# Kernel optimization log

Measured on AMD Instinct MI355X. Metric: run time of the kernel, lower is better.

The kernel has to match this reference:

```python
import jax, jax.numpy as jnp
import numpy as np

N, E, F_IN, D, H = 20000, 640000, 128, 16, 8  # nodes, edges, in_features, out_features, n_heads


def _linear_params(k, fan_in, fan_out):
    W = jax.random.normal(k, (fan_in, fan_out), jnp.float32) / np.sqrt(fan_in)
    b = jnp.zeros((fan_out,), jnp.float32)
    return W, b


def setup_inputs() -> dict:
    key = jax.random.key(0)
    ks = jax.random.split(key, 8)
    x = jax.random.normal(ks[0], (N, F_IN), jnp.float32)
    edge_index = jax.random.randint(ks[1], (2, E), 0, N, dtype=jnp.int64)
    Wq, bq = _linear_params(ks[2], F_IN, D * H)
    Wk, bk = _linear_params(ks[3], F_IN, D * H)
    Wv, bv = _linear_params(ks[4], F_IN, D * H)
    Wpsi, bpsi = _linear_params(ks[5], D, D)
    Wo, bo = _linear_params(ks[6], D * H * 2, F_IN)
    gamma = jnp.ones((F_IN,), jnp.float32)
    beta = jnp.zeros((F_IN,), jnp.float32)
    return {"x": x, "edge_index": edge_index, "Wq": Wq, "bq": bq, "Wk": Wk, "bk": bk,
            "Wv": Wv, "bv": bv, "Wpsi": Wpsi, "bpsi": bpsi, "Wo": Wo, "bo": bo,
            "gamma": gamma, "beta": beta}


def _segment_softmax(logits, seg, num_segments):
    # numerically-stable softmax of edge logits grouped by destination node (row)
    m = jax.ops.segment_max(logits, seg, num_segments=num_segments)  # [N,H]
    m = jnp.where(jnp.isfinite(m), m, 0.0)
    e = jnp.exp(logits - m[seg])  # [E,H]
    s = jax.ops.segment_sum(e, seg, num_segments=num_segments)  # [N,H]
    return e / (s[seg] + 1e-16)


def reference(x, edge_index, Wq, bq, Wk, bk, Wv, bv, Wpsi, bpsi, Wo, bo, gamma, beta):
    q = (x @ Wq + bq).reshape(N, H, D)
    k = (x @ Wk + bk).reshape(N, H, D)
    v = (x @ Wv + bv).reshape(N, H, D)
    row, col = edge_index[0], edge_index[1]

    logits = jnp.einsum('ehd,ehd->eh', q[row], k[col]) / np.sqrt(D)  # [E,H]
    alpha = _segment_softmax(logits, row, N)  # [E,H]

    v_j = v[col]  # [E,H,D]
    h_lp = jax.ops.segment_sum((alpha[..., None] * v_j).reshape(E, H * D), row, num_segments=N)
    v_bp = jnp.tanh(v_j @ Wpsi + bpsi)  # per-head linear on last dim, [E,H,D]
    h_bp = jax.ops.segment_sum((alpha[..., None] * v_bp).reshape(E, H * D), row, num_segments=N)

    h_out = jnp.concatenate([h_lp, h_bp], axis=1) @ Wo + bo  # [N,F_IN]
    y = x + jax.nn.relu(h_out)
    mu = jnp.mean(y, axis=-1, keepdims=True)
    var = jnp.mean(jnp.square(y - mu), axis=-1, keepdims=True)
    return (y - mu) * jax.lax.rsqrt(var + 1e-5) * gamma + beta
```

## Files before the change

### kernel.cpp

```cpp
#include <hip/hip_runtime.h>
#include <hip/hip_bf16.h>
#include <math.h>

#define NN 20000
#define EE 640000
#define NCH 8
#define CHN 2500
#define SLOT 24

typedef __attribute__((ext_vector_type(8))) short short8;
typedef __attribute__((ext_vector_type(4))) float f32x4;
typedef __hip_bfloat16 bf16;
typedef __hip_bfloat162 bf162;

__device__ inline ushort f2bf(float f) {
  bf16 h = __float2bfloat16(f);
  return *(ushort*)&h;
}
__device__ inline float2 ldbf2(const ushort* p) {
  return __bfloat1622float2(*(const bf162*)p);
}
__device__ inline float2 bf2u(uint u) {
  return __bfloat1622float2(*(const bf162*)&u);
}
__device__ inline float fast_tanh(float x) {
  float xx = fminf(fmaxf(x, -9.0f), 9.0f);
  float e = exp2f(xx * 2.885390082f);
  return (e - 1.0f) * __builtin_amdgcn_rcpf(e + 1.0f);
}


__global__ __launch_bounds__(256) void qkv_mfma(
    const float* __restrict__ x,
    const float* __restrict__ Wq, const float* __restrict__ bq,
    const float* __restrict__ Wk, const float* __restrict__ bk,
    const float* __restrict__ Wv, const float* __restrict__ bv,
    const float* __restrict__ Wpsi, const float* __restrict__ bpsi,
    float* __restrict__ qbuf, ushort* __restrict__ kvb,
    int* __restrict__ cursor2) {
  __shared__ ushort As[128 * 136];
  __shared__ ushort Bts[128 * 136];
  __shared__ float Wps[256];
  __shared__ float bps[16];
  int t = threadIdx.x;
  {
    int flat = (blockIdx.y * 157 + blockIdx.x) * 256 + t;
    for (int j = flat; j < NN * NCH; j += 157 * 3 * 256) cursor2[j] = 0;
  }
  int n0 = blockIdx.x * 128;
  int mat = blockIdx.y;
  const float* W    = mat == 0 ? Wq : (mat == 1 ? Wk : Wv);
  const float* bias = mat == 0 ? bq : (mat == 1 ? bk : bv);
  if (mat == 2) {
    Wps[t] = Wpsi[t];
    if (t < 16) bps[t] = bpsi[t];
  }

  {
    int r = t >> 1, half = (t & 1) * 64;
    int n = n0 + r;
    ushort* dst = &As[r * 136 + half];
    if (n < NN) {
      const float* src = x + (size_t)n * 128 + half;
#pragma unroll
      for (int j = 0; j < 8; ++j) {
        float4 f0 = *(const float4*)(src + 8 * j);
        float4 f1 = *(const float4*)(src + 8 * j + 4);
        ushort tmp[8] = {f2bf(f0.x), f2bf(f0.y), f2bf(f0.z), f2bf(f0.w),
                         f2bf(f1.x), f2bf(f1.y), f2bf(f1.z), f2bf(f1.w)};
        *(uint4*)(dst + 8 * j) = *(uint4*)tmp;
      }
    } else {
#pragma unroll
      for (int j = 0; j < 8; ++j) *(uint4*)(dst + 8 * j) = make_uint4(0, 0, 0, 0);
    }
  }
  {
    int k = t >> 1, nh = (t & 1) * 64;
    const float* src = W + (size_t)k * 128 + nh;
#pragma unroll
    for (int i = 0; i < 16; ++i) {
      float4 f = *(const float4*)(src + 4 * i);
      Bts[(nh + 4 * i + 0) * 136 + k] = f2bf(f.x);
      Bts[(nh + 4 * i + 1) * 136 + k] = f2bf(f.y);
      Bts[(nh + 4 * i + 2) * 136 + k] = f2bf(f.z);
      Bts[(nh + 4 * i + 3) * 136 + k] = f2bf(f.w);
    }
  }
  __syncthreads();

  int w = t >> 6, lane = t & 63;
  int m = lane & 15, q = lane >> 4;
  int r0 = w * 32;
  f32x4 acc0[8], acc1[8];
#pragma unroll
  for (int c = 0; c < 8; ++c) {
    acc0[c] = (f32x4){0.f, 0.f, 0.f, 0.f};
    acc1[c] = (f32x4){0.f, 0.f, 0.f, 0.f};
  }
#pragma unroll
  for (int kb = 0; kb < 4; ++kb) {
    int kof = kb * 32 + 8 * q;
    short8 a0 = *(const short8*)&As[(r0 + m) * 136 + kof];
    short8 a1 = *(const short8*)&As[(r0 + 16 + m) * 136 + kof];
#pragma unroll
    for (int c = 0; c < 8; ++c) {
      short8 b = *(const short8*)&Bts[(c * 16 + m) * 136 + kof];
      acc0[c] = __builtin_amdgcn_mfma_f32_16x16x32_bf16(a0, b, acc0[c], 0, 0, 0);
      acc1[c] = __builtin_amdgcn_mfma_f32_16x16x32_bf16(a1, b, acc1[c], 0, 0, 0);
    }
  }
  if (mat == 2) __syncthreads();

  int koff2 = (mat == 2) ? 4 : 0;
#pragma unroll
  for (int c = 0; c < 8; ++c) {
    int col = c * 16 + m;
    float bb = bias[col];
    size_t pos = (size_t)(c * 4 + (m >> 2)) * 12 + (m & 3) + koff2;
#pragma unroll
    for (int reg = 0; reg < 4; ++reg) {
      int rl0 = r0 + 4 * q + reg;
      int rl1 = rl0 + 16;
      int row0 = n0 + rl0;
      int row1 = n0 + rl1;
      float v0 = acc0[c][reg] + bb;
      float v1 = acc1[c][reg] + bb;
      if (mat == 0) {
        if (row0 < NN) qbuf[(size_t)row0 * 128 + col] = v0;
        if (row1 < NN) qbuf[(size_t)row1 * 128 + col] = v1;
      } else {
        if (row0 < NN) kvb[(size_t)row0 * 384 + pos] = f2bf(v0);
        if (row1 < NN) kvb[(size_t)row1 * 384 + pos] = f2bf(v1);
        if (mat == 2) {
          Bts[rl0 * 136 + col] = f2bf(v0);
          Bts[rl1 * 136 + col] = f2bf(v1);
        }
      }
    }
  }

  if (mat == 2) {
    __syncthreads();
#pragma unroll
    for (int ii = 0; ii < 4; ++ii) {
      int idx = ii * 256 + t;
      int rloc = idx >> 3, h = idx & 7;
      int n = n0 + rloc;
      const ushort* vp = &Bts[rloc * 136 + h * 16];
      uint4 a = *(const uint4*)vp;
      uint4 b = *(const uint4*)(vp + 8);
      float v[16];
      {
        float2 f;
        f = bf2u(a.x); v[0] = f.x;  v[1] = f.y;
        f = bf2u(a.y); v[2] = f.x;  v[3] = f.y;
        f = bf2u(a.z); v[4] = f.x;  v[5] = f.y;
        f = bf2u(a.w); v[6] = f.x;  v[7] = f.y;
        f = bf2u(b.x); v[8] = f.x;  v[9] = f.y;
        f = bf2u(b.y); v[10] = f.x; v[11] = f.y;
        f = bf2u(b.z); v[12] = f.x; v[13] = f.y;
        f = bf2u(b.w); v[14] = f.x; v[15] = f.y;
      }
      float o[16];
#pragma unroll
      for (int d = 0; d < 16; ++d) o[d] = bps[d];
#pragma unroll
      for (int dp = 0; dp < 16; ++dp) {
        float vv = v[dp];
#pragma unroll
        for (int d = 0; d < 16; ++d) o[d] = fmaf(vv, Wps[dp * 16 + d], o[d]);
      }
      if (n < NN) {
        ushort* dst = kvb + (size_t)n * 384;
#pragma unroll
        for (int j = 0; j < 8; ++j) {
          uint u = (uint)f2bf(fast_tanh(o[2 * j])) |
                   ((uint)f2bf(fast_tanh(o[2 * j + 1])) << 16);
          int grp = h * 4 + (j >> 1);
          int within = (2 * j) & 3;
          *(uint*)(dst + grp * 12 + 8 + within) = u;
        }
      }
    }
  }
}

__global__ __launch_bounds__(256) void scatter_kernel(
    const int* __restrict__ ei,
    int* __restrict__ cursor2, ushort* __restrict__ scol2) {
  int e = blockIdx.x * 256 + threadIdx.x;
  if (e < EE) {
    int r = ei[e];
    int c = ei[EE + e];
    int ch = c / CHN;
    int pos = atomicAdd(&cursor2[r * NCH + ch], 1);
    if (pos < SLOT) scol2[(r * NCH + ch) * SLOT + pos] = (ushort)c;
  }
}

__global__ __launch_bounds__(256) void aggregate_kernel(
    const float* __restrict__ qbuf, const ushort* __restrict__ kvb,
    const int* __restrict__ cursor2, const ushort* __restrict__ scol2,
    ushort* __restrict__ hbufb) {
  int t = threadIdx.x;
  int lane = t & 63;
  int wid = __builtin_amdgcn_readfirstlane(t >> 6);
  int wg = blockIdx.x * 4 + wid;
  int n0 = wg * 2;
  int l31 = lane & 31;
  int half = lane >> 5;
  const float SC = 0.25f * 1.44269504f;

  float4 q0 = *(const float4*)(qbuf + (size_t)n0 * 128 + l31 * 4);
  float4 q1 = *(const float4*)(qbuf + (size_t)(n0 + 1) * 128 + l31 * 4);
  q0.x *= SC; q0.y *= SC; q0.z *= SC; q0.w *= SC;
  q1.x *= SC; q1.y *= SC; q1.z *= SC; q1.w *= SC;

  int mycnt = cursor2[n0 * NCH + (lane & 15)];

  float s0 = 0.f, s1 = 0.f;
  float4 aV0 = make_float4(0.f, 0.f, 0.f, 0.f), aV1 = aV0;
  float4 aB0 = aV0, aB1 = aV0;

  const char* kvc = (const char*)kvb;
  uint lo24 = (uint)l31 * 24u;

  for (int ch = 0; ch < NCH; ++ch) {
#pragma unroll
    for (int ni = 0; ni < 2; ++ni) {
      int cnt = __builtin_amdgcn_readfirstlane(__shfl(mycnt, ni * NCH + ch));
      cnt = cnt > SLOT ? SLOT : cnt;
      if (cnt == 0) continue;
      const uint* slu = (const uint*)(scol2 + ((n0 + ni) * NCH + ch) * SLOT);
      float4 q = ni ? q1 : q0;
      float ls = 0.f;
      float4 lV = make_float4(0.f, 0.f, 0.f, 0.f);
      float4 lB = make_float4(0.f, 0.f, 0.f, 0.f);
      int npair = (cnt + 1) >> 1;
      for (int p = 0; p < npair; ++p) {
        uint wv = slu[p];
        uint e0 = wv & 0xffffu;
        uint e1 = wv >> 16;
        bool pv = (2 * p + 1) < cnt;
        uint e1c = pv ? e1 : e0;
        uint e = half ? e1c : e0;
        const char* pb = kvc + (size_t)e * 768u + lo24;
        uint4 L0 = *(const uint4*)pb;
        uint2 L1 = *(const uint2*)(pb + 16);
        float2 k0 = bf2u(L0.x), k1 = bf2u(L0.y);
        float d = fmaf(q.x, k0.x, fmaf(q.y, k0.y, fmaf(q.z, k1.x, q.w * k1.y)));
        d += __shfl_xor(d, 1);
        d += __shfl_xor(d, 2);
        float wgt = exp2f(d);
        wgt = (half && !pv) ? 0.f : wgt;
        ls += wgt;
        float2 v0 = bf2u(L0.z), v1 = bf2u(L0.w);
        lV.x = fmaf(wgt, v0.x, lV.x); lV.y = fmaf(wgt, v0.y, lV.y);
        lV.z = fmaf(wgt, v1.x, lV.z); lV.w = fmaf(wgt, v1.y, lV.w);
        float2 b0 = bf2u(L1.x), b1 = bf2u(L1.y);
        lB.x = fmaf(wgt, b0.x, lB.x); lB.y = fmaf(wgt, b0.y, lB.y);
        lB.z = fmaf(wgt, b1.x, lB.z); lB.w = fmaf(wgt, b1.y, lB.w);
      }
      if (ni == 0) {
        s0 += ls;
        aV0.x += lV.x; aV0.y += lV.y; aV0.z += lV.z; aV0.w += lV.w;
        aB0.x += lB.x; aB0.y += lB.y; aB0.z += lB.z; aB0.w += lB.w;
      } else {
        s1 += ls;
        aV1.x += lV.x; aV1.y += lV.y; aV1.z += lV.z; aV1.w += lV.w;
        aB1.x += lB.x; aB1.y += lB.y; aB1.z += lB.z; aB1.w += lB.w;
      }
    }
    __syncthreads();
  }

#pragma unroll
  for (int ni = 0; ni < 2; ++ni) {
    float s = ni ? s1 : s0;
    float4 V = ni ? aV1 : aV0;
    float4 B = ni ? aB1 : aB0;
    s += __shfl_xor(s, 32);
    V.x += __shfl_xor(V.x, 32); V.y += __shfl_xor(V.y, 32);
    V.z += __shfl_xor(V.z, 32); V.w += __shfl_xor(V.w, 32);
    B.x += __shfl_xor(B.x, 32); B.y += __shfl_xor(B.y, 32);
    B.z += __shfl_xor(B.z, 32); B.w += __shfl_xor(B.w, 32);
    float inv = s > 0.f ? 1.f / s : 0.f;
    if (half == 0) {
      ushort* hp = hbufb + (size_t)(n0 + ni) * 256 + l31 * 4;
      uint2 uv, ub;
      uv.x = (uint)f2bf(V.x * inv) | ((uint)f2bf(V.y * inv) << 16);
      uv.y = (uint)f2bf(V.z * inv) | ((uint)f2bf(V.w * inv) << 16);
      ub.x = (uint)f2bf(B.x * inv) | ((uint)f2bf(B.y * inv) << 16);
      ub.y = (uint)f2bf(B.z * inv) | ((uint)f2bf(B.w * inv) << 16);
      *(uint2*)(hp)       = uv;
      *(uint2*)(hp + 128) = ub;
    }
  }
}

__global__ __launch_bounds__(256) void output_mfma(
    const ushort* __restrict__ hbufb, const float* __restrict__ x,
    const float* __restrict__ Wo, const float* __restrict__ bo,
    const float* __restrict__ gamma, const float* __restrict__ beta,
    float* __restrict__ out) {
  __shared__ ushort As[128 * 136];
  __shared__ ushort Bts[128 * 136];
  __shared__ float bos[128], gs[128], bts[128];
  int t = threadIdx.x;
  int n0 = blockIdx.x * 128;
  if (t < 128) { bos[t] = bo[t]; gs[t] = gamma[t]; bts[t] = beta[t]; }
  int w = t >> 6, lane = t & 63;
  int m = lane & 15, q = lane >> 4;
  int r0 = w * 32;
  f32x4 acc0[8], acc1[8];
#pragma unroll
  for (int c = 0; c < 8; ++c) {
    acc0[c] = (f32x4){0.f, 0.f, 0.f, 0.f};
    acc1[c] = (f32x4){0.f, 0.f, 0.f, 0.f};
  }
  for (int kc = 0; kc < 2; ++kc) {
    if (kc) __syncthreads();
    {
      int r = t >> 1, half = (t & 1) * 64;
      int n = n0 + r;
      ushort* dst = &As[r * 136 + half];
      if (n < NN) {
        const ushort* src = hbufb + (size_t)n * 256 + kc * 128 + half;
#pragma unroll
        for (int j = 0; j < 8; ++j)
          *(uint4*)(dst + 8 * j) = *(const uint4*)(src + 8 * j);
      } else {
#pragma unroll
        for (int j = 0; j < 8; ++j) *(uint4*)(dst + 8 * j) = make_uint4(0, 0, 0, 0);
      }
    }
    {
      int k = t >> 1, nh = (t & 1) * 64;
      const float* src = Wo + (size_t)(kc * 128 + k) * 128 + nh;
#pragma unroll
      for (int i = 0; i < 16; ++i) {
        float4 f = *(const float4*)(src + 4 * i);
        Bts[(nh + 4 * i + 0) * 136 + k] = f2bf(f.x);
        Bts[(nh + 4 * i + 1) * 136 + k] = f2bf(f.y);
        Bts[(nh + 4 * i + 2) * 136 + k] = f2bf(f.z);
        Bts[(nh + 4 * i + 3) * 136 + k] = f2bf(f.w);
      }
    }
    __syncthreads();
#pragma unroll
    for (int kb = 0; kb < 4; ++kb) {
      int kof = kb * 32 + 8 * q;
      short8 a0 = *(const short8*)&As[(r0 + m) * 136 + kof];
      short8 a1 = *(const short8*)&As[(r0 + 16 + m) * 136 + kof];
#pragma unroll
      for (int c = 0; c < 8; ++c) {
        short8 b = *(const short8*)&Bts[(c * 16 + m) * 136 + kof];
        acc0[c] = __builtin_amdgcn_mfma_f32_16x16x32_bf16(a0, b, acc0[c], 0, 0, 0);
        acc1[c] = __builtin_amdgcn_mfma_f32_16x16x32_bf16(a1, b, acc1[c], 0, 0, 0);
      }
    }
  }
#pragma unroll
  for (int half = 0; half < 2; ++half) {
#pragma unroll
    for (int reg = 0; reg < 4; ++reg) {
      int row = n0 + r0 + half * 16 + 4 * q + reg;
      bool valid = row < NN;
      float vals[8];
      float sum = 0.f;
#pragma unroll
      for (int c = 0; c < 8; ++c) {
        int col = c * 16 + m;
        float a = (half ? acc1[c][reg] : acc0[c][reg]) + bos[col];
        a = fmaxf(a, 0.f);
        float xv = valid ? x[(size_t)row * 128 + col] : 0.f;
        float v = a + xv;
        vals[c] = v;
        sum += v;
      }
      sum += __shfl_xor(sum, 1); sum += __shfl_xor(sum, 2);
      sum += __shfl_xor(sum, 4); sum += __shfl_xor(sum, 8);
      float mean = sum * (1.f / 128.f);
      float ssq = 0.f;
#pragma unroll
      for (int c = 0; c < 8; ++c) {
        float d = vals[c] - mean;
        ssq = fmaf(d, d, ssq);
      }
      ssq += __shfl_xor(ssq, 1); ssq += __shfl_xor(ssq, 2);
      ssq += __shfl_xor(ssq, 4); ssq += __shfl_xor(ssq, 8);
      float rstd = rsqrtf(ssq * (1.f / 128.f) + 1e-5f);
      if (valid) {
#pragma unroll
        for (int c = 0; c < 8; ++c) {
          int col = c * 16 + m;
          out[(size_t)row * 128 + col] = (vals[c] - mean) * rstd * gs[col] + bts[col];
        }
      }
    }
  }
}

extern "C" void kernel_launch(void* const* d_in, const int* in_sizes, int n_in,
                              void* d_out, int out_size, void* d_ws, size_t ws_size,
                              hipStream_t stream) {
  const float* x     = (const float*)d_in[0];
  const int*   ei    = (const int*)d_in[1];
  const float* Wq    = (const float*)d_in[2];
  const float* bq    = (const float*)d_in[3];
  const float* Wk    = (const float*)d_in[4];
  const float* bk    = (const float*)d_in[5];
  const float* Wv    = (const float*)d_in[6];
  const float* bv    = (const float*)d_in[7];
  const float* Wpsi  = (const float*)d_in[8];
  const float* bpsi  = (const float*)d_in[9];
  const float* Wo    = (const float*)d_in[10];
  const float* bo    = (const float*)d_in[11];
  const float* gamma = (const float*)d_in[12];
  const float* beta  = (const float*)d_in[13];
  float* out = (float*)d_out;

  char* ws = (char*)d_ws;
  float*  qbuf    = (float*) (ws);
  ushort* kvb     = (ushort*)(ws + 10240000);
  ushort* hbufb   = (ushort*)(ws + 25600000);
  int*    cursor2 = (int*)   (ws + 35840000);
  ushort* scol2   = (ushort*)(ws + 36480000);

  qkv_mfma<<<dim3(157, 3), 256, 0, stream>>>(x, Wq, bq, Wk, bk, Wv, bv,
                                             Wpsi, bpsi, qbuf, kvb, cursor2);
  scatter_kernel<<<2500, 256, 0, stream>>>(ei, cursor2, scol2);
  aggregate_kernel<<<2500, 256, 0, stream>>>(qbuf, kvb, cursor2, scol2, hbufb);
  output_mfma<<<157, 256, 0, stream>>>(hbufb, x, Wo, bo, gamma, beta, out);
}
```

Baseline: 233.8 us.

## Fuse K and V projections per block, stage kvb rows in LDS, interleave aggregation nodes

Measured after the change: 275.6 us. 1.18x slower.

```diff
diff --git a/kernel.cpp b/kernel.cpp
--- a/kernel.cpp
+++ b/kernel.cpp
@@ -38,20 +38,20 @@
     const float* __restrict__ Wpsi, const float* __restrict__ bpsi,
     float* __restrict__ qbuf, ushort* __restrict__ kvb,
     int* __restrict__ cursor2) {
-  __shared__ ushort As[128 * 136];
-  __shared__ ushort Bts[128 * 136];
+  __shared__ ushort SM[34816];
   __shared__ float Wps[256];
   __shared__ float bps[16];
+  ushort* As = SM;
+  ushort* WB = SM + 17408;
+  ushort* Rs = SM;
   int t = threadIdx.x;
   {
     int flat = (blockIdx.y * 157 + blockIdx.x) * 256 + t;
-    for (int j = flat; j < NN * NCH; j += 157 * 3 * 256) cursor2[j] = 0;
+    for (int j = flat; j < NN * NCH; j += 157 * 2 * 256) cursor2[j] = 0;
   }
   int n0 = blockIdx.x * 128;
   int mat = blockIdx.y;
-  const float* W    = mat == 0 ? Wq : (mat == 1 ? Wk : Wv);
-  const float* bias = mat == 0 ? bq : (mat == 1 ? bk : bv);
-  if (mat == 2) {
+  if (mat == 1) {
     Wps[t] = Wpsi[t];
     if (t < 16) bps[t] = bpsi[t];
   }
@@ -75,92 +75,117 @@
       for (int j = 0; j < 8; ++j) *(uint4*)(dst + 8 * j) = make_uint4(0, 0, 0, 0);
     }
   }
-  {
+  auto stageW = [&](const float* W) {
     int k = t >> 1, nh = (t & 1) * 64;
     const float* src = W + (size_t)k * 128 + nh;
 #pragma unroll
     for (int i = 0; i < 16; ++i) {
       float4 f = *(const float4*)(src + 4 * i);
-      Bts[(nh + 4 * i + 0) * 136 + k] = f2bf(f.x);
-      Bts[(nh + 4 * i + 1) * 136 + k] = f2bf(f.y);
-      Bts[(nh + 4 * i + 2) * 136 + k] = f2bf(f.z);
-      Bts[(nh + 4 * i + 3) * 136 + k] = f2bf(f.w);
-    }
-  }
-  __syncthreads();
+      WB[(nh + 4 * i + 0) * 136 + k] = f2bf(f.x);
+      WB[(nh + 4 * i + 1) * 136 + k] = f2bf(f.y);
+      WB[(nh + 4 * i + 2) * 136 + k] = f2bf(f.z);
+      WB[(nh + 4 * i + 3) * 136 + k] = f2bf(f.w);
+    }
+  };
 
   int w = t >> 6, lane = t & 63;
   int m = lane & 15, q = lane >> 4;
   int r0 = w * 32;
-  f32x4 acc0[8], acc1[8];
+
+  auto runMFMA = [&](f32x4 (&a0)[8], f32x4 (&a1)[8]) {
+#pragma unroll
+    for (int kb = 0; kb < 4; ++kb) {
+      int kof = kb * 32 + 8 * q;
+      short8 x0 = *(const short8*)&As[(r0 + m) * 136 + kof];
+      short8 x1 = *(const short8*)&As[(r0 + 16 + m) * 136 + kof];
+#pragma unroll
+      for (int c = 0; c < 8; ++c) {
+        short8 b = *(const short8*)&WB[(c * 16 + m) * 136 + kof];
+        a0[c] = __builtin_amdgcn_mfma_f32_16x16x32_bf16(x0, b, a0[c], 0, 0, 0);
+        a1[c] = __builtin_amdgcn_mfma_f32_16x16x32_bf16(x1, b, a1[c], 0, 0, 0);
+      }
+    }
+  };
+
+  if (mat == 0) {
+    stageW(Wq);
+    __syncthreads();
+    f32x4 acc0[8], acc1[8];
+#pragma unroll
+    for (int c = 0; c < 8; ++c) {
+      acc0[c] = (f32x4){0.f, 0.f, 0.f, 0.f};
+      acc1[c] = (f32x4){0.f, 0.f, 0.f, 0.f};
+    }
+    runMFMA(acc0, acc1);
+#pragma unroll
+    for (int c = 0; c < 8; ++c) {
+      int col = c * 16 + m;
+      float bb = bq[col];
+#pragma unroll
+      for (int reg = 0; reg < 4; ++reg) {
+        int row0 = n0 + r0 + 4 * q + reg;
+        int row1 = row0 + 16;
+        if (row0 < NN) qbuf[(size_t)row0 * 128 + col] = acc0[c][reg] + bb;
+        if (row1 < NN) qbuf[(size_t)row1 * 128 + col] = acc1[c][reg] + bb;
+      }
+    }
+    return;
+  }
+
+  stageW(Wk);
+  __syncthreads();
+  f32x4 ak0[8], ak1[8], av0[8], av1[8];
 #pragma unroll
   for (int c = 0; c < 8; ++c) {
-    acc0[c] = (f32x4){0.f, 0.f, 0.f, 0.f};
-    acc1[c] = (f32x4){0.f, 0.f, 0.f, 0.f};
-  }
-#pragma unroll
-  for (int kb = 0; kb < 4; ++kb) {
-    int kof = kb * 32 + 8 * q;
-    short8 a0 = *(const short8*)&As[(r0 + m) * 136 + kof];
-    short8 a1 = *(const short8*)&As[(r0 + 16 + m) * 136 + kof];
-#pragma unroll
-    for (int c = 0; c < 8; ++c) {
-      short8 b = *(const short8*)&Bts[(c * 16 + m) * 136 + kof];
-      acc0[c] = __builtin_amdgcn_mfma_f32_16x16x32_bf16(a0, b, acc0[c], 0, 0, 0);
-      acc1[c] = __builtin_amdgcn_mfma_f32_16x16x32_bf16(a1, b, acc1[c], 0, 0, 0);
-    }
-  }
-  if (mat == 2) __syncthreads();
-
-  int koff2 = (mat == 2) ? 4 : 0;
+    ak0[c] = (f32x4){0.f, 0.f, 0.f, 0.f};
+    ak1[c] = (f32x4){0.f, 0.f, 0.f, 0.f};
+    av0[c] = (f32x4){0.f, 0.f, 0.f, 0.f};
+    av1[c] = (f32x4){0.f, 0.f, 0.f, 0.f};
+  }
+  runMFMA(ak0, ak1);
+  __syncthreads();
+  stageW(Wv);
+  __syncthreads();
+  runMFMA(av0, av1);
+  __syncthreads();
+
+  float bbk[8], bbv[8];
 #pragma unroll
   for (int c = 0; c < 8; ++c) {
-    int col = c * 16 + m;
-    float bb = bias[col];
-    size_t pos = (size_t)(c * 4 + (m >> 2)) * 12 + (m & 3) + koff2;
-#pragma unroll
-    for (int reg = 0; reg < 4; ++reg) {
-      int rl0 = r0 + 4 * q + reg;
-      int rl1 = rl0 + 16;
-      int row0 = n0 + rl0;
-      int row1 = n0 + rl1;
-      float v0 = acc0[c][reg] + bb;
-      float v1 = acc1[c][reg] + bb;
-      if (mat == 0) {
-        if (row0 < NN) qbuf[(size_t)row0 * 128 + col] = v0;
-        if (row1 < NN) qbuf[(size_t)row1 * 128 + col] = v1;
-      } else {
-        if (row0 < NN) kvb[(size_t)row0 * 384 + pos] = f2bf(v0);
-        if (row1 < NN) kvb[(size_t)row1 * 384 + pos] = f2bf(v1);
-        if (mat == 2) {
-          Bts[rl0 * 136 + col] = f2bf(v0);
-          Bts[rl1 * 136 + col] = f2bf(v1);
+    bbk[c] = bk[c * 16 + m];
+    bbv[c] = bv[c * 16 + m];
+  }
+
+#pragma unroll
+  for (int hf = 0; hf < 2; ++hf) {
+    if (hf) __syncthreads();
+    if ((w >> 1) == hf) {
+      int rbase = (w & 1) * 32;
+#pragma unroll
+      for (int c = 0; c < 8; ++c) {
+        int gof = (c * 4 + (m >> 2)) * 12 + (m & 3);
+#pragma unroll
+        for (int reg = 0; reg < 4; ++reg) {
+          int rl = rbase + 4 * q + reg;
+          Rs[rl * 392 + gof]            = f2bf(ak0[c][reg] + bbk[c]);
+          Rs[rl * 392 + gof + 4]        = f2bf(av0[c][reg] + bbv[c]);
+          Rs[(rl + 16) * 392 + gof]     = f2bf(ak1[c][reg] + bbk[c]);
+          Rs[(rl + 16) * 392 + gof + 4] = f2bf(av1[c][reg] + bbv[c]);
         }
       }
     }
-  }
-
-  if (mat == 2) {
     __syncthreads();
 #pragma unroll
-    for (int ii = 0; ii < 4; ++ii) {
-      int idx = ii * 256 + t;
-      int rloc = idx >> 3, h = idx & 7;
-      int n = n0 + rloc;
-      const ushort* vp = &Bts[rloc * 136 + h * 16];
-      uint4 a = *(const uint4*)vp;
-      uint4 b = *(const uint4*)(vp + 8);
+    for (int ii = 0; ii < 2; ++ii) {
+      int cell = ii * 256 + t;
+      int rl = cell >> 3, h = cell & 7;
       float v[16];
-      {
-        float2 f;
-        f = bf2u(a.x); v[0] = f.x;  v[1] = f.y;
-        f = bf2u(a.y); v[2] = f.x;  v[3] = f.y;
-        f = bf2u(a.z); v[4] = f.x;  v[5] = f.y;
-        f = bf2u(a.w); v[6] = f.x;  v[7] = f.y;
-        f = bf2u(b.x); v[8] = f.x;  v[9] = f.y;
-        f = bf2u(b.y); v[10] = f.x; v[11] = f.y;
-        f = bf2u(b.z); v[12] = f.x; v[13] = f.y;
-        f = bf2u(b.w); v[14] = f.x; v[15] = f.y;
+#pragma unroll
+      for (int dq = 0; dq < 4; ++dq) {
+        const ushort* vp = &Rs[rl * 392 + (h * 4 + dq) * 12 + 4];
+        float2 f0 = ldbf2(vp), f1 = ldbf2(vp + 2);
+        v[4 * dq] = f0.x; v[4 * dq + 1] = f0.y;
+        v[4 * dq + 2] = f1.x; v[4 * dq + 3] = f1.y;
       }
       float o[16];
 #pragma unroll
@@ -171,16 +196,24 @@
 #pragma unroll
         for (int d = 0; d < 16; ++d) o[d] = fmaf(vv, Wps[dp * 16 + d], o[d]);
       }
+#pragma unroll
+      for (int dq = 0; dq < 4; ++dq) {
+        uint u0 = (uint)f2bf(fast_tanh(o[4 * dq])) |
+                  ((uint)f2bf(fast_tanh(o[4 * dq + 1])) << 16);
+        uint u1 = (uint)f2bf(fast_tanh(o[4 * dq + 2])) |
+                  ((uint)f2bf(fast_tanh(o[4 * dq + 3])) << 16);
+        *(uint2*)&Rs[rl * 392 + (h * 4 + dq) * 12 + 8] = make_uint2(u0, u1);
+      }
+    }
+    __syncthreads();
+#pragma unroll
+    for (int i = 0; i < 12; ++i) {
+      int flat = i * 256 + t;
+      int rl = flat / 48, of = flat % 48;
+      int n = n0 + hf * 64 + rl;
       if (n < NN) {
-        ushort* dst = kvb + (size_t)n * 384;
-#pragma unroll
-        for (int j = 0; j < 8; ++j) {
-          uint u = (uint)f2bf(fast_tanh(o[2 * j])) |
-                   ((uint)f2bf(fast_tanh(o[2 * j + 1])) << 16);
-          int grp = h * 4 + (j >> 1);
-          int within = (2 * j) & 3;
-          *(uint*)(dst + grp * 12 + 8 + within) = u;
-        }
+        uint4 d = *(const uint4*)&Rs[rl * 392 + of * 8];
+        *(uint4*)(kvb + (size_t)n * 384 + of * 8) = d;
       }
     }
   }
@@ -227,52 +260,58 @@
   uint lo24 = (uint)l31 * 24u;
 
   for (int ch = 0; ch < NCH; ++ch) {
-#pragma unroll
-    for (int ni = 0; ni < 2; ++ni) {
-      int cnt = __builtin_amdgcn_readfirstlane(__shfl(mycnt, ni * NCH + ch));
-      cnt = cnt > SLOT ? SLOT : cnt;
-      if (cnt == 0) continue;
-      const uint* slu = (const uint*)(scol2 + ((n0 + ni) * NCH + ch) * SLOT);
-      float4 q = ni ? q1 : q0;
-      float ls = 0.f;
-      float4 lV = make_float4(0.f, 0.f, 0.f, 0.f);
-      float4 lB = make_float4(0.f, 0.f, 0.f, 0.f);
-      int npair = (cnt + 1) >> 1;
-      for (int p = 0; p < npair; ++p) {
-        uint wv = slu[p];
-        uint e0 = wv & 0xffffu;
-        uint e1 = wv >> 16;
-        bool pv = (2 * p + 1) < cnt;
-        uint e1c = pv ? e1 : e0;
-        uint e = half ? e1c : e0;
-        const char* pb = kvc + (size_t)e * 768u + lo24;
-        uint4 L0 = *(const uint4*)pb;
-        uint2 L1 = *(const uint2*)(pb + 16);
+    int c0 = __builtin_amdgcn_readfirstlane(__shfl(mycnt, ch));
+    int c1 = __builtin_amdgcn_readfirstlane(__shfl(mycnt, 8 + ch));
+    c0 = c0 > SLOT ? SLOT : c0;
+    c1 = c1 > SLOT ? SLOT : c1;
+    int np0 = (c0 + 1) >> 1, np1 = (c1 + 1) >> 1;
+    int npm = np0 > np1 ? np0 : np1;
+    if (npm == 0) continue;
+    const uint* slu0 = (const uint*)(scol2 + ((size_t)n0 * NCH + ch) * SLOT);
+    const uint* slu1 = (const uint*)(scol2 + ((size_t)(n0 + 1) * NCH + ch) * SLOT);
+    for (int p = 0; p < npm; ++p) {
+      uint wv0 = (p < np0) ? slu0[p] : 0u;
+      uint wv1 = (p < np1) ? slu1[p] : 0u;
+      bool o0 = (2 * p + 1) < c0, o1 = (2 * p + 1) < c1;
+      uint e0 = half ? (o0 ? (wv0 >> 16) : (wv0 & 0xffffu)) : (wv0 & 0xffffu);
+      uint e1 = half ? (o1 ? (wv1 >> 16) : (wv1 & 0xffffu)) : (wv1 & 0xffffu);
+      bool v0 = (2 * p + half) < c0;
+      bool v1 = (2 * p + half) < c1;
+      const char* pb0 = kvc + (size_t)e0 * 768u + lo24;
+      const char* pb1 = kvc + (size_t)e1 * 768u + lo24;
+      uint4 L0 = *(const uint4*)pb0;
+      uint2 M0 = *(const uint2*)(pb0 + 16);
+      uint4 L1 = *(const uint4*)pb1;
+      uint2 M1 = *(const uint2*)(pb1 + 16);
+      {
         float2 k0 = bf2u(L0.x), k1 = bf2u(L0.y);
-        float d = fmaf(q.x, k0.x, fmaf(q.y, k0.y, fmaf(q.z, k1.x, q.w * k1.y)));
+        float d = fmaf(q0.x, k0.x, fmaf(q0.y, k0.y, fmaf(q0.z, k1.x, q0.w * k1.y)));
         d += __shfl_xor(d, 1);
         d += __shfl_xor(d, 2);
-        float wgt = exp2f(d);
-        wgt = (half && !pv) ? 0.f : wgt;
-        ls += wgt;
-        float2 v0 = bf2u(L0.z), v1 = bf2u(L0.w);
-        lV.x = fmaf(wgt, v0.x, lV.x); lV.y = fmaf(wgt, v0.y, lV.y);
-        lV.z = fmaf(wgt, v1.x, lV.z); lV.w = fmaf(wgt, v1.y, lV.w);
-        float2 b0 = bf2u(L1.x), b1 = bf2u(L1.y);
-        lB.x = fmaf(wgt, b0.x, lB.x); lB.y = fmaf(wgt, b0.y, lB.y);
-        lB.z = fmaf(wgt, b1.x, lB.z); lB.w = fmaf(wgt, b1.y, lB.w);
-      }
-      if (ni == 0) {
-        s0 += ls;
-        aV0.x += lV.x; aV0.y += lV.y; aV0.z += lV.z; aV0.w += lV.w;
-        aB0.x += lB.x; aB0.y += lB.y; aB0.z += lB.z; aB0.w += lB.w;
-      } else {
-        s1 += ls;
-        aV1.x += lV.x; aV1.y += lV.y; aV1.z += lV.z; aV1.w += lV.w;
-        aB1.x += lB.x; aB1.y += lB.y; aB1.z += lB.z; aB1.w += lB.w;
-      }
-    }
-    __syncthreads();
+        float wgt = v0 ? exp2f(d) : 0.f;
+        s0 += wgt;
+        float2 vv0 = bf2u(L0.z), vv1 = bf2u(L0.w);
+        aV0.x = fmaf(wgt, vv0.x, aV0.x); aV0.y = fmaf(wgt, vv0.y, aV0.y);
+        aV0.z = fmaf(wgt, vv1.x, aV0.z); aV0.w = fmaf(wgt, vv1.y, aV0.w);
+        float2 b0 = bf2u(M0.x), b1 = bf2u(M0.y);
+        aB0.x = fmaf(wgt, b0.x, aB0.x); aB0.y = fmaf(wgt, b0.y, aB0.y);
+        aB0.z = fmaf(wgt, b1.x, aB0.z); aB0.w = fmaf(wgt, b1.y, aB0.w);
+      }
+      {
+        float2 k0 = bf2u(L1.x), k1 = bf2u(L1.y);
+        float d = fmaf(q1.x, k0.x, fmaf(q1.y, k0.y, fmaf(q1.z, k1.x, q1.w * k1.y)));
+        d += __shfl_xor(d, 1);
+        d += __shfl_xor(d, 2);
+        float wgt = v1 ? exp2f(d) : 0.f;
+        s1 += wgt;
+        float2 vv0 = bf2u(L1.z), vv1 = bf2u(L1.w);
+        aV1.x = fmaf(wgt, vv0.x, aV1.x); aV1.y = fmaf(wgt, vv0.y, aV1.y);
+        aV1.z = fmaf(wgt, vv1.x, aV1.z); aV1.w = fmaf(wgt, vv1.y, aV1.w);
+        float2 b0 = bf2u(M1.x), b1 = bf2u(M1.y);
+        aB1.x = fmaf(wgt, b0.x, aB1.x); aB1.y = fmaf(wgt, b0.y, aB1.y);
+        aB1.z = fmaf(wgt, b1.x, aB1.z); aB1.w = fmaf(wgt, b1.y, aB1.w);
+      }
+    }
   }
 
 #pragma unroll
@@ -428,7 +467,7 @@
   int*    cursor2 = (int*)   (ws + 35840000);
   ushort* scol2   = (ushort*)(ws + 36480000);
 
-  qkv_mfma<<<dim3(157, 3), 256, 0, stream>>>(x, Wq, bq, Wk, bk, Wv, bv,
+  qkv_mfma<<<dim3(157, 2), 256, 0, stream>>>(x, Wq, bq, Wk, bk, Wv, bv,
                                              Wpsi, bpsi, qbuf, kvb, cursor2);
   scatter_kernel<<<2500, 256, 0, stream>>>(ei, cursor2, scol2);
   aggregate_kernel<<<2500, 256, 0, stream>>>(qbuf, kvb, cursor2, scol2, hbufb);
```
